# Optimization experiments

Measured on AMD Instinct MI355X. Metric: run time of the kernel, lower is better.

The kernel has to match this reference:

```python
import jax, jax.numpy as jnp
import numpy as np

BIT_SHIFT = 4
PROJECT = True
DIMS = [4096, 4096, 4096, 4096]
BATCH = 8192


def ternarize(w):
    # Ternary weight quantization {-1,0,+1} with straight-through estimator.
    q = jnp.clip(jnp.round(w), -1.0, 1.0)
    return w + jax.lax.stop_gradient(q - w)


def binarize(x):
    # Binary projection sign(x) with hardtanh straight-through estimator.
    c = jnp.clip(x, -1.0, 1.0)
    return c + jax.lax.stop_gradient(jnp.sign(x) - c)


def tern_bin_layer(x, w):
    # Ternary-weight matmul followed by bit-shift scaling (divide by 2**BIT_SHIFT),
    # then optional binary projection of the activation.
    scale = 1.0 / (1 << BIT_SHIFT)
    y = jnp.matmul(x, ternarize(w)) * scale
    if PROJECT:
        y = binarize(y)
    return y


def setup_inputs() -> dict:
    key = jax.random.key(0)
    ks = jax.random.split(key, 4)
    x = jax.random.normal(ks[0], (BATCH, DIMS[0]), dtype=jnp.float32)
    # Latent float weights; ternarized inside the layer.
    W0 = jax.random.normal(ks[1], (DIMS[0], DIMS[1]), dtype=jnp.float32) * 0.7
    W1 = jax.random.normal(ks[2], (DIMS[1], DIMS[2]), dtype=jnp.float32) * 0.7
    W2 = jax.random.normal(ks[3], (DIMS[2], DIMS[3]), dtype=jnp.float32) * 0.7
    return {"x": x, "W0": W0, "W1": W1, "W2": W2}


def reference(x, W0, W1, W2):
    h = tern_bin_layer(x, W0)
    h = tern_bin_layer(h, W1)
    h = tern_bin_layer(h, W2)
    return h
```

## Files before the change

### kernel.cpp

```cpp
#include <hip/hip_runtime.h>
#include <stdint.h>

#define MDIM 8192
#define KDIM 4096
#define NDIM 4096
#define MAXFLAGS (2 * 1024 * 1024)

typedef int i32x4 __attribute__((ext_vector_type(4)));

#define VMCNT(n) asm volatile("s_waitcnt vmcnt(" #n ")" ::: "memory")
#define LGKMCNT0 asm volatile("s_waitcnt lgkmcnt(0)" ::: "memory")
#define SB0 __builtin_amdgcn_sched_barrier(0)

__device__ __forceinline__ void gl2lds16(const void* g, void* l) {
  __builtin_amdgcn_global_load_lds(
      (const __attribute__((address_space(1))) void*)(uintptr_t)(g),
      (__attribute__((address_space(3))) void*)(uintptr_t)(l), 16, 0, 0);
}

__global__ __launch_bounds__(256) void k_tern(const float* __restrict__ W,
                                              int8_t* __restrict__ Qt) {
  __shared__ int8_t t[64][65];
  const int n0 = blockIdx.x * 64;
  const int k0 = blockIdx.y * 64;
  const int tid = threadIdx.x;
  const int c = tid & 63;
  const int r0 = tid >> 6;
#pragma unroll
  for (int i = 0; i < 16; ++i) {
    int r = (i << 2) + r0;
    float w = W[(size_t)(k0 + r) * NDIM + (n0 + c)];
    float q = fminf(1.f, fmaxf(-1.f, rintf(w)));
    t[r][c] = (int8_t)(int)q;
  }
  __syncthreads();
#pragma unroll
  for (int i = 0; i < 16; ++i) {
    int r = (i << 2) + r0;
    Qt[(size_t)(n0 + r) * KDIM + (k0 + c)] = t[c][r];
  }
}

__global__ __launch_bounds__(256) void k_quant(const float* __restrict__ x,
                                               int8_t* __restrict__ dig) {
  const size_t P = (size_t)MDIM * KDIM;
  size_t i = ((size_t)blockIdx.x * 256 + threadIdx.x) * 4;
  float4 v = *(const float4*)(x + i);
  float f[4] = {v.x, v.y, v.z, v.w};
  int8_t dd[3][4];
#pragma unroll
  for (int j = 0; j < 4; ++j) {
    long long s = __double2ll_rn((double)f[j] * 524288.0);
    int8_t d0 = (int8_t)s; s = (s - d0) >> 8;
    int8_t d1 = (int8_t)s; s = (s - d1) >> 8;
    int8_t d2 = (int8_t)s;
    dd[0][j] = d0; dd[1][j] = d1; dd[2][j] = d2;
  }
#pragma unroll
  for (int p = 0; p < 3; ++p) {
    char4 c4; c4.x = dd[p][0]; c4.y = dd[p][1]; c4.z = dd[p][2]; c4.w = dd[p][3];
    *(char4*)(dig + p * P + i) = c4;
  }
}

__global__ void k_zero(int* c) {
  if (threadIdx.x == 0 && blockIdx.x == 0) *c = 0;
}

__global__ __launch_bounds__(512) void k_gemm_l1(const int8_t* __restrict__ dig,
                                                 const int8_t* __restrict__ Qt,
                                                 int8_t* __restrict__ h,
                                                 int* __restrict__ cnt,
                                                 int2* __restrict__ flags) {
  __shared__ __align__(16) int8_t As[2][3][64][128];
  __shared__ __align__(16) int8_t Bs[2][128][128];
  const int tid = threadIdx.x;
  const int w = tid >> 6, l = tid & 63;
  const size_t P = (size_t)MDIM * KDIM;

  const int nwg = gridDim.x;
  const int wg = (blockIdx.x & 7) * (nwg >> 3) + (blockIdx.x >> 3);
  const int NB = NDIM / 128;
  const int mb = wg / NB, nb = wg % NB;

  const int srow = tid >> 3;
  const int sswz = (tid & 7) ^ (srow & 7);
  const int8_t* a_src = dig + (size_t)(mb * 64 + srow) * KDIM + sswz * 16;
  const int8_t* b_src0 = Qt + (size_t)(nb * 128 + srow) * KDIM + sswz * 16;
  const int8_t* b_src1 = b_src0 + (size_t)64 * KDIM;

  i32x4 acc[3][2][2];
#pragma unroll
  for (int p = 0; p < 3; ++p)
#pragma unroll
    for (int mi = 0; mi < 2; ++mi)
#pragma unroll
      for (int ni = 0; ni < 2; ++ni) acc[p][mi][ni] = (i32x4){0, 0, 0, 0};

  const int wr = (w >> 2) * 32;
  const int wc = (w & 3) * 32;

  auto stage = [&](int buf, int kk) {
    int8_t* ad = &As[buf][0][0][0] + w * 1024;
    int8_t* bd = &Bs[buf][0][0] + w * 1024;
#pragma unroll
    for (int p = 0; p < 3; ++p) gl2lds16(a_src + p * P + kk, ad + p * 8192);
    gl2lds16(b_src0 + kk, bd);
    gl2lds16(b_src1 + kk, bd + 8192);
  };

  auto compute = [&](int buf) {
#pragma unroll
    for (int ki = 0; ki < 2; ++ki) {
      const int kg = ki * 4 + (l >> 4);
      i32x4 b[2];
#pragma unroll
      for (int ni = 0; ni < 2; ++ni) {
        int nr = wc + ni * 16 + (l & 15);
        b[ni] = *(const i32x4*)&Bs[buf][nr][(kg ^ (nr & 7)) * 16];
      }
      __builtin_amdgcn_s_setprio(1);
#pragma unroll
      for (int p = 0; p < 3; ++p)
#pragma unroll
        for (int mi = 0; mi < 2; ++mi) {
          int ar = wr + mi * 16 + (l & 15);
          i32x4 a = *(const i32x4*)&As[buf][p][ar][(kg ^ (ar & 7)) * 16];
#pragma unroll
          for (int ni = 0; ni < 2; ++ni)
            acc[p][mi][ni] =
                __builtin_amdgcn_mfma_i32_16x16x64_i8(a, b[ni], acc[p][mi][ni], 0, 0, 0);
        }
      __builtin_amdgcn_s_setprio(0);
    }
  };

  stage(0, 0);
  stage(1, 128);
  VMCNT(5);
  SB0;
  __builtin_amdgcn_s_barrier();

  const int NT = KDIM / 128;
  for (int t = 0; t < NT; ++t) {
    compute(t & 1);
    if (t == NT - 1) break;
    LGKMCNT0; SB0;
    __builtin_amdgcn_s_barrier();
    if (t + 2 < NT) {
      stage(t & 1, (t + 2) * 128);
      VMCNT(5);
    } else {
      VMCNT(0);
    }
    SB0;
    __builtin_amdgcn_s_barrier();
  }

  const int mbase = mb * 64 + wr + ((l >> 4) << 2);
  const int nbase = nb * 128 + wc + (l & 15);
#pragma unroll
  for (int mi = 0; mi < 2; ++mi)
#pragma unroll
    for (int ni = 0; ni < 2; ++ni)
#pragma unroll
      for (int j = 0; j < 4; ++j) {
        int s0 = acc[0][mi][ni][j], s1 = acc[1][mi][ni][j];
        int s2 = acc[2][mi][ni][j];
        double d = ((double)s2 * 256.0 + (double)s1) * 256.0 + (double)s0;
        int sg = (d > 0.0) - (d < 0.0);
        int row = mbase + mi * 16 + j;
        int col = nbase + ni * 16;
        h[(size_t)row * NDIM + col] = (int8_t)sg;
        if (fabs(d) <= 2048.0) {
          int idx = atomicAdd(cnt, 1);
          if (idx < MAXFLAGS) flags[idx] = make_int2(row, col);
        }
      }
}

__global__ __launch_bounds__(256) void k_fixup(const float* __restrict__ x,
                                               const int8_t* __restrict__ Qt,
                                               const int* __restrict__ cnt,
                                               const int2* __restrict__ flags,
                                               int8_t* __restrict__ h) {
  __shared__ double red[256];
  int n = *cnt;
  if (n > MAXFLAGS) n = MAXFLAGS;
  for (int i = blockIdx.x; i < n; i += gridDim.x) {
    int2 rc = flags[i];
    const float* xr = x + (size_t)rc.x * KDIM;
    const int8_t* qr = Qt + (size_t)rc.y * KDIM;
    double s = 0.0;
    for (int k = threadIdx.x; k < KDIM; k += 256)
      s += (double)xr[k] * (double)qr[k];
    red[threadIdx.x] = s;
    __syncthreads();
#pragma unroll
    for (int st = 128; st > 0; st >>= 1) {
      if (threadIdx.x < st) red[threadIdx.x] += red[threadIdx.x + st];
      __syncthreads();
    }
    if (threadIdx.x == 0) {
      double d = red[0];
      h[(size_t)rc.x * NDIM + rc.y] = (int8_t)((d > 0.0) - (d < 0.0));
    }
    __syncthreads();
  }
}

template <int F32OUT>
__global__ __launch_bounds__(512, 2) void k_gemm_bin(const int8_t* __restrict__ A,
                                                     const int8_t* __restrict__ Qt,
                                                     void* __restrict__ outp) {
  __shared__ __align__(16) int8_t smem[131072];
  const int tid = threadIdx.x;
  const int w = tid >> 6, l = tid & 63;

  const int nwg = gridDim.x;
  const int wg = (blockIdx.x & 7) * (nwg >> 3) + (blockIdx.x >> 3);
  const int NB = NDIM / 256;
  const int mb = wg / NB, nb = wg % NB;

  const int cs = ((l & 7) ^ ((l >> 3) & 7)) << 4;
  const int r0 = w * 32 + (l >> 3);
  const int8_t* gA[4];
  const int8_t* gB[4];
#pragma unroll
  for (int s = 0; s < 4; ++s) {
    gA[s] = A + (size_t)(mb * 256 + r0 + s * 8) * KDIM + cs;
    gB[s] = Qt + (size_t)(nb * 256 + r0 + s * 8) * KDIM + cs;
  }
  const int dA = w * 4096 + l * 16;

  i32x4 acc[8][4];
#pragma unroll
  for (int mi = 0; mi < 8; ++mi)
#pragma unroll
    for (int ni = 0; ni < 4; ++ni) acc[mi][ni] = (i32x4){0, 0, 0, 0};

  const int wr = (w >> 2) * 128, wc = (w & 3) * 64;

  auto stage = [&](int buf, int kk) {
    int8_t* sb = smem + buf * 65536;
#pragma unroll
    for (int s = 0; s < 4; ++s) gl2lds16(gA[s] + kk, sb + dA + s * 1024);
#pragma unroll
    for (int s = 0; s < 4; ++s) gl2lds16(gB[s] + kk, sb + 32768 + dA + s * 1024);
  };

  auto compute = [&](int buf) {
    const int8_t* sb = smem + buf * 65536;
#pragma unroll
    for (int ki = 0; ki < 2; ++ki) {
      const int kg = ki * 4 + (l >> 4);
      i32x4 b[4], a[8];
#pragma unroll
      for (int ni = 0; ni < 4; ++ni) {
        int nr = wc + ni * 16 + (l & 15);
        b[ni] = *(const i32x4*)(sb + 32768 + nr * 128 + ((kg ^ (nr & 7)) << 4));
      }
#pragma unroll
      for (int mi = 0; mi < 8; ++mi) {
        int ar = wr + mi * 16 + (l & 15);
        a[mi] = *(const i32x4*)(sb + ar * 128 + ((kg ^ (ar & 7)) << 4));
      }
      __builtin_amdgcn_s_setprio(1);
#pragma unroll
      for (int mi = 0; mi < 8; ++mi)
#pragma unroll
        for (int ni = 0; ni < 4; ++ni)
          acc[mi][ni] =
              __builtin_amdgcn_mfma_i32_16x16x64_i8(a[mi], b[ni], acc[mi][ni], 0, 0, 0);
      __builtin_amdgcn_s_setprio(0);
    }
  };

  const int NT = KDIM / 128;
  stage(0, 0); stage(1, 128);
  VMCNT(8);
  SB0;
  __builtin_amdgcn_s_barrier();

  for (int t = 0; t < NT; ++t) {
    compute(t & 1);
    if (t == NT - 1) break;
    LGKMCNT0; SB0;
    __builtin_amdgcn_s_barrier();
    if (t + 2 < NT) {
      stage(t & 1, (t + 2) * 128);
      VMCNT(8);
    } else {
      VMCNT(0);
    }
    SB0;
    __builtin_amdgcn_s_barrier();
  }

  const int mbase = mb * 256 + wr + ((l >> 4) << 2);
  const int nbase = nb * 256 + wc + (l & 15);
#pragma unroll
  for (int mi = 0; mi < 8; ++mi)
#pragma unroll
    for (int ni = 0; ni < 4; ++ni)
#pragma unroll
      for (int j = 0; j < 4; ++j) {
        int s = acc[mi][ni][j];
        int sg = (s > 0) - (s < 0);
        size_t off = (size_t)(mbase + mi * 16 + j) * NDIM + (nbase + ni * 16);
        if (F32OUT)
          ((float*)outp)[off] = (float)sg;
        else
          ((int8_t*)outp)[off] = (int8_t)sg;
      }
}

extern "C" void kernel_launch(void* const* d_in, const int* in_sizes, int n_in,
                              void* d_out, int out_size, void* d_ws, size_t ws_size,
                              hipStream_t stream) {
  (void)in_sizes; (void)n_in; (void)out_size; (void)ws_size;
  const float* x  = (const float*)d_in[0];
  const float* W0 = (const float*)d_in[1];
  const float* W1 = (const float*)d_in[2];
  const float* W2 = (const float*)d_in[3];
  float* out = (float*)d_out;

  const size_t QB = (size_t)KDIM * NDIM;
  const size_t HB = (size_t)MDIM * NDIM;
  int8_t* Qt0 = (int8_t*)d_ws;
  int8_t* Qt1 = Qt0 + QB;
  int8_t* Qt2 = Qt1 + QB;
  int8_t* h0  = Qt2 + QB;
  int8_t* h1  = h0 + HB;

  int8_t* dig = (int8_t*)d_out;
  int2* flags = (int2*)((char*)d_out + 3 * HB);
  int* cnt = (int*)((char*)d_out + 3 * HB + (size_t)MAXFLAGS * 8);

  dim3 tgrid(NDIM / 64, KDIM / 64);
  k_tern<<<tgrid, 256, 0, stream>>>(W0, Qt0);
  k_tern<<<tgrid, 256, 0, stream>>>(W1, Qt1);
  k_tern<<<tgrid, 256, 0, stream>>>(W2, Qt2);
  k_quant<<<((size_t)MDIM * KDIM) / 1024, 256, 0, stream>>>(x, dig);
  k_zero<<<1, 64, 0, stream>>>(cnt);
  k_gemm_l1<<<(MDIM / 64) * (NDIM / 128), 512, 0, stream>>>(dig, Qt0, h0, cnt, flags);
  k_fixup<<<512, 256, 0, stream>>>(x, Qt0, cnt, flags, h0);
  k_gemm_bin<0><<<(MDIM / 256) * (NDIM / 256), 512, 0, stream>>>(h0, Qt1, h1);
  k_gemm_bin<1><<<(MDIM / 256) * (NDIM / 256), 512, 0, stream>>>(h1, Qt2, out);
}
```

Before: 753.5 us.

## Enlarge layer-1 int8 GEMM tile to 128x256 and fuse prep kernels

The first-layer three-plane int8 GEMM goes from a 64x128 block tile to a 128x256 tile. Each wave now computes a 64x64 sub-tile with 4x4 MFMA fragments per digit plane, and the double-buffered LDS grows to 160KB. This raises arithmetic intensity per byte loaded and cuts how often each A and B tile is reloaded. The cost is a large accumulator register footprint and one block per CU. Separately, the three ternarize-transpose kernels, the input digit-quantize kernel and the counter reset merge into one vectorized launch, removing several launches.

```diff
diff --git a/kernel.cpp b/kernel.cpp
--- a/kernel.cpp
+++ b/kernel.cpp
@@ -18,130 +18,155 @@
       (__attribute__((address_space(3))) void*)(uintptr_t)(l), 16, 0, 0);
 }
 
-__global__ __launch_bounds__(256) void k_tern(const float* __restrict__ W,
-                                              int8_t* __restrict__ Qt) {
-  __shared__ int8_t t[64][65];
-  const int n0 = blockIdx.x * 64;
-  const int k0 = blockIdx.y * 64;
+__global__ __launch_bounds__(256) void k_prep(const float* __restrict__ x,
+                                              const float* __restrict__ W0,
+                                              const float* __restrict__ W1,
+                                              const float* __restrict__ W2,
+                                              int8_t* __restrict__ Qt0,
+                                              int8_t* __restrict__ Qt1,
+                                              int8_t* __restrict__ Qt2,
+                                              int8_t* __restrict__ dig,
+                                              int* __restrict__ cnt) {
+  const int bid = blockIdx.x;
   const int tid = threadIdx.x;
-  const int c = tid & 63;
-  const int r0 = tid >> 6;
-#pragma unroll
-  for (int i = 0; i < 16; ++i) {
-    int r = (i << 2) + r0;
-    float w = W[(size_t)(k0 + r) * NDIM + (n0 + c)];
-    float q = fminf(1.f, fmaxf(-1.f, rintf(w)));
-    t[r][c] = (int8_t)(int)q;
-  }
-  __syncthreads();
-#pragma unroll
-  for (int i = 0; i < 16; ++i) {
-    int r = (i << 2) + r0;
-    Qt[(size_t)(n0 + r) * KDIM + (k0 + c)] = t[c][r];
-  }
-}
-
-__global__ __launch_bounds__(256) void k_quant(const float* __restrict__ x,
-                                               int8_t* __restrict__ dig) {
-  const size_t P = (size_t)MDIM * KDIM;
-  size_t i = ((size_t)blockIdx.x * 256 + threadIdx.x) * 4;
-  float4 v = *(const float4*)(x + i);
-  float f[4] = {v.x, v.y, v.z, v.w};
-  int8_t dd[3][4];
-#pragma unroll
-  for (int j = 0; j < 4; ++j) {
-    long long s = __double2ll_rn((double)f[j] * 524288.0);
-    int8_t d0 = (int8_t)s; s = (s - d0) >> 8;
-    int8_t d1 = (int8_t)s; s = (s - d1) >> 8;
-    int8_t d2 = (int8_t)s;
-    dd[0][j] = d0; dd[1][j] = d1; dd[2][j] = d2;
-  }
-#pragma unroll
-  for (int p = 0; p < 3; ++p) {
-    char4 c4; c4.x = dd[p][0]; c4.y = dd[p][1]; c4.z = dd[p][2]; c4.w = dd[p][3];
-    *(char4*)(dig + p * P + i) = c4;
-  }
-}
-
-__global__ void k_zero(int* c) {
-  if (threadIdx.x == 0 && blockIdx.x == 0) *c = 0;
-}
-
-__global__ __launch_bounds__(512) void k_gemm_l1(const int8_t* __restrict__ dig,
-                                                 const int8_t* __restrict__ Qt,
-                                                 int8_t* __restrict__ h,
-                                                 int* __restrict__ cnt,
-                                                 int2* __restrict__ flags) {
-  __shared__ __align__(16) int8_t As[2][3][64][128];
-  __shared__ __align__(16) int8_t Bs[2][128][128];
+  if (bid == 0 && tid == 0) *cnt = 0;
+  if (bid < 12288) {
+    __shared__ int8_t t[64][68];
+    const int wsel = bid >> 12;
+    const int r = bid & 4095;
+    const int n0 = (r & 63) * 64, k0 = (r >> 6) * 64;
+    const float* W = (wsel == 0) ? W0 : (wsel == 1) ? W1 : W2;
+    int8_t* Qt = (wsel == 0) ? Qt0 : (wsel == 1) ? Qt1 : Qt2;
+    const int c4 = tid & 15, rq = tid >> 4;
+#pragma unroll
+    for (int i = 0; i < 4; ++i) {
+      int row = i * 16 + rq;
+      float4 v = *(const float4*)&W[(size_t)(k0 + row) * NDIM + n0 + c4 * 4];
+      float f[4] = {v.x, v.y, v.z, v.w};
+#pragma unroll
+      for (int j = 0; j < 4; ++j) {
+        float q = fminf(1.f, fmaxf(-1.f, rintf(f[j])));
+        t[row][c4 * 4 + j] = (int8_t)(int)q;
+      }
+    }
+    __syncthreads();
+#pragma unroll
+    for (int i = 0; i < 4; ++i) {
+      int n = i * 16 + rq;
+      char4 o;
+      o.x = t[c4 * 4 + 0][n];
+      o.y = t[c4 * 4 + 1][n];
+      o.z = t[c4 * 4 + 2][n];
+      o.w = t[c4 * 4 + 3][n];
+      *(char4*)&Qt[(size_t)(n0 + n) * KDIM + k0 + c4 * 4] = o;
+    }
+  } else {
+    const size_t P = (size_t)MDIM * KDIM;
+    size_t i = ((size_t)(bid - 12288) * 256 + tid) * 4;
+    float4 v = *(const float4*)(x + i);
+    float f[4] = {v.x, v.y, v.z, v.w};
+    int8_t dd[3][4];
+#pragma unroll
+    for (int j = 0; j < 4; ++j) {
+      long long s = __double2ll_rn((double)f[j] * 524288.0);
+      int8_t d0 = (int8_t)s; s = (s - d0) >> 8;
+      int8_t d1 = (int8_t)s; s = (s - d1) >> 8;
+      int8_t d2 = (int8_t)s;
+      dd[0][j] = d0; dd[1][j] = d1; dd[2][j] = d2;
+    }
+#pragma unroll
+    for (int p = 0; p < 3; ++p) {
+      char4 c4v; c4v.x = dd[p][0]; c4v.y = dd[p][1]; c4v.z = dd[p][2]; c4v.w = dd[p][3];
+      *(char4*)(dig + p * P + i) = c4v;
+    }
+  }
+}
+
+__global__ __launch_bounds__(512, 2) void k_gemm_l1(const int8_t* __restrict__ dig,
+                                                    const int8_t* __restrict__ Qt,
+                                                    int8_t* __restrict__ h,
+                                                    int* __restrict__ cnt,
+                                                    int2* __restrict__ flags) {
+  __shared__ __align__(16) int8_t smem[163840];
   const int tid = threadIdx.x;
   const int w = tid >> 6, l = tid & 63;
   const size_t P = (size_t)MDIM * KDIM;
 
   const int nwg = gridDim.x;
   const int wg = (blockIdx.x & 7) * (nwg >> 3) + (blockIdx.x >> 3);
-  const int NB = NDIM / 128;
+  const int NB = NDIM / 256;
   const int mb = wg / NB, nb = wg % NB;
 
-  const int srow = tid >> 3;
-  const int sswz = (tid & 7) ^ (srow & 7);
-  const int8_t* a_src = dig + (size_t)(mb * 64 + srow) * KDIM + sswz * 16;
-  const int8_t* b_src0 = Qt + (size_t)(nb * 128 + srow) * KDIM + sswz * 16;
-  const int8_t* b_src1 = b_src0 + (size_t)64 * KDIM;
-
-  i32x4 acc[3][2][2];
+  const int cs = ((l & 7) ^ ((l >> 3) & 7)) << 4;
+  const int8_t* gsrc[10];
+  int doff[10];
+#pragma unroll
+  for (int s = 0; s < 10; ++s) {
+    int i = w + 8 * s;
+    if (i < 48) {
+      int arow = i * 8 + (l >> 3);
+      gsrc[s] = dig + (size_t)(arow >> 7) * P + (size_t)(mb * 128 + (arow & 127)) * KDIM + cs;
+    } else {
+      int brow = (i - 48) * 8 + (l >> 3);
+      gsrc[s] = Qt + (size_t)(nb * 256 + brow) * KDIM + cs;
+    }
+    doff[s] = i * 1024 + l * 16;
+  }
+
+  i32x4 acc[3][4][4];
 #pragma unroll
   for (int p = 0; p < 3; ++p)
 #pragma unroll
-    for (int mi = 0; mi < 2; ++mi)
-#pragma unroll
-      for (int ni = 0; ni < 2; ++ni) acc[p][mi][ni] = (i32x4){0, 0, 0, 0};
-
-  const int wr = (w >> 2) * 32;
-  const int wc = (w & 3) * 32;
+    for (int mi = 0; mi < 4; ++mi)
+#pragma unroll
+      for (int ni = 0; ni < 4; ++ni) acc[p][mi][ni] = (i32x4){0, 0, 0, 0};
+
+  const int wr = (w >> 2) * 64;
+  const int wc = (w & 3) * 64;
 
   auto stage = [&](int buf, int kk) {
-    int8_t* ad = &As[buf][0][0][0] + w * 1024;
-    int8_t* bd = &Bs[buf][0][0] + w * 1024;
-#pragma unroll
-    for (int p = 0; p < 3; ++p) gl2lds16(a_src + p * P + kk, ad + p * 8192);
-    gl2lds16(b_src0 + kk, bd);
-    gl2lds16(b_src1 + kk, bd + 8192);
+    int8_t* sb = smem + buf * 81920;
+#pragma unroll
+    for (int s = 0; s < 10; ++s) gl2lds16(gsrc[s] + kk, sb + doff[s]);
   };
 
   auto compute = [&](int buf) {
+    const int8_t* sb = smem + buf * 81920;
 #pragma unroll
     for (int ki = 0; ki < 2; ++ki) {
       const int kg = ki * 4 + (l >> 4);
-      i32x4 b[2];
-#pragma unroll
-      for (int ni = 0; ni < 2; ++ni) {
+      i32x4 b[4];
+#pragma unroll
+      for (int ni = 0; ni < 4; ++ni) {
         int nr = wc + ni * 16 + (l & 15);
-        b[ni] = *(const i32x4*)&Bs[buf][nr][(kg ^ (nr & 7)) * 16];
-      }
-      __builtin_amdgcn_s_setprio(1);
-#pragma unroll
-      for (int p = 0; p < 3; ++p)
-#pragma unroll
-        for (int mi = 0; mi < 2; ++mi) {
+        b[ni] = *(const i32x4*)(sb + 49152 + nr * 128 + ((kg ^ (nr & 7)) << 4));
+      }
+#pragma unroll
+      for (int p = 0; p < 3; ++p) {
+        i32x4 a[4];
+#pragma unroll
+        for (int mi = 0; mi < 4; ++mi) {
           int ar = wr + mi * 16 + (l & 15);
-          i32x4 a = *(const i32x4*)&As[buf][p][ar][(kg ^ (ar & 7)) * 16];
-#pragma unroll
-          for (int ni = 0; ni < 2; ++ni)
+          a[mi] = *(const i32x4*)(sb + p * 16384 + ar * 128 + ((kg ^ (ar & 7)) << 4));
+        }
+        __builtin_amdgcn_s_setprio(1);
+#pragma unroll
+        for (int mi = 0; mi < 4; ++mi)
+#pragma unroll
+          for (int ni = 0; ni < 4; ++ni)
             acc[p][mi][ni] =
-                __builtin_amdgcn_mfma_i32_16x16x64_i8(a, b[ni], acc[p][mi][ni], 0, 0, 0);
-        }
-      __builtin_amdgcn_s_setprio(0);
+                __builtin_amdgcn_mfma_i32_16x16x64_i8(a[mi], b[ni], acc[p][mi][ni], 0, 0, 0);
+        __builtin_amdgcn_s_setprio(0);
+      }
     }
   };
 
-  stage(0, 0);
-  stage(1, 128);
-  VMCNT(5);
+  const int NT = KDIM / 128;
+  stage(0, 0); stage(1, 128);
+  VMCNT(10);
   SB0;
   __builtin_amdgcn_s_barrier();
 
-  const int NT = KDIM / 128;
   for (int t = 0; t < NT; ++t) {
     compute(t & 1);
     if (t == NT - 1) break;
@@ -149,7 +174,7 @@
     __builtin_amdgcn_s_barrier();
     if (t + 2 < NT) {
       stage(t & 1, (t + 2) * 128);
-      VMCNT(5);
+      VMCNT(10);
     } else {
       VMCNT(0);
     }
@@ -157,12 +182,12 @@
     __builtin_amdgcn_s_barrier();
   }
 
-  const int mbase = mb * 64 + wr + ((l >> 4) << 2);
-  const int nbase = nb * 128 + wc + (l & 15);
-#pragma unroll
-  for (int mi = 0; mi < 2; ++mi)
-#pragma unroll
-    for (int ni = 0; ni < 2; ++ni)
+  const int mbase = mb * 128 + wr + ((l >> 4) << 2);
+  const int nbase = nb * 256 + wc + (l & 15);
+#pragma unroll
+  for (int mi = 0; mi < 4; ++mi)
+#pragma unroll
+    for (int ni = 0; ni < 4; ++ni)
 #pragma unroll
       for (int j = 0; j < 4; ++j) {
         int s0 = acc[0][mi][ni][j], s1 = acc[1][mi][ni][j];
@@ -337,13 +362,8 @@
   int2* flags = (int2*)((char*)d_out + 3 * HB);
   int* cnt = (int*)((char*)d_out + 3 * HB + (size_t)MAXFLAGS * 8);
 
-  dim3 tgrid(NDIM / 64, KDIM / 64);
-  k_tern<<<tgrid, 256, 0, stream>>>(W0, Qt0);
-  k_tern<<<tgrid, 256, 0, stream>>>(W1, Qt1);
-  k_tern<<<tgrid, 256, 0, stream>>>(W2, Qt2);
-  k_quant<<<((size_t)MDIM * KDIM) / 1024, 256, 0, stream>>>(x, dig);
-  k_zero<<<1, 64, 0, stream>>>(cnt);
-  k_gemm_l1<<<(MDIM / 64) * (NDIM / 128), 512, 0, stream>>>(dig, Qt0, h0, cnt, flags);
+  k_prep<<<45056, 256, 0, stream>>>(x, W0, W1, W2, Qt0, Qt1, Qt2, dig, cnt);
+  k_gemm_l1<<<(MDIM / 128) * (NDIM / 256), 512, 0, stream>>>(dig, Qt0, h0, cnt, flags);
   k_fixup<<<512, 256, 0, stream>>>(x, Qt0, cnt, flags, h0);
   k_gemm_bin<0><<<(MDIM / 256) * (NDIM / 256), 512, 0, stream>>>(h0, Qt1, h1);
   k_gemm_bin<1><<<(MDIM / 256) * (NDIM / 256), 512, 0, stream>>>(h1, Qt2, out);
```

Result: slower. 846.4 us (+12.3%).
